# Kernel optimization log

Hardware: AMD Instinct MI355X
Metric: run time of the kernel (lower is better)

## Reference

```python
import jax, jax.numpy as jnp
import numpy as np

B, N, D, H, M = 4, 4096, 1024, 16, 128
DH = D // H
SCALE = DH ** -0.5


def setup_inputs() -> dict:
    key = jax.random.key(0)
    k1, k2, k3, k4, k5 = jax.random.split(key, 5)
    return {
        "x": jax.random.normal(k1, (B, N, D), dtype=jnp.float32),
        "agent_tokens": jax.random.normal(k2, (H, M, DH), dtype=jnp.float32) * 0.02,
        "w_fused": jax.random.normal(k3, (3 * D, D), dtype=jnp.float32) * 0.02,
        "w_qa": jax.random.normal(k4, (H, H), dtype=jnp.float32) * 0.25,
        "w_ak": jax.random.normal(k5, (H, H), dtype=jnp.float32) * 0.25,
    }


def reference(x, agent_tokens, w_fused, w_qa, w_ak):
    b, n, d = x.shape
    # Fused QKV projection (torch Linear: x @ W.T), split into q, k, v
    qkv = jnp.einsum('bnd,ed->bne', x, w_fused)  # [B, N, 3D]
    q, k, v = jnp.split(qkv, 3, axis=-1)
    # [B, N, (H dh)] -> [B, H, N, dh]
    def to_heads(t):
        return t.reshape(b, n, H, DH).transpose(0, 2, 1, 3)
    q, k, v = to_heads(q), to_heads(k), to_heads(v)
    a = agent_tokens * SCALE  # [H, M, dh], broadcast over batch
    # Stage 1 scores: query -> agents ; agents -> keys
    qa_attn = jax.nn.softmax(jnp.einsum('bhnd,hmd->bhnm', q, a), axis=-1)  # [B,H,N,M]
    ak_attn = jax.nn.softmax(jnp.einsum('hmd,bhnd->bhmn', a, k), axis=-1)  # [B,H,M,N]
    # Talking heads: 1x1 conv over head dim == HxH mixing matrix
    qa_attn = jnp.einsum('gh,bhnm->bgnm', w_qa, qa_attn)
    ak_attn = jnp.einsum('gh,bhmn->bgmn', w_ak, ak_attn)
    # Two-stage value aggregation
    agent_gathered = jnp.einsum('bhmn,bhnd->bhmd', ak_attn, v)   # [B,H,M,dh]
    out = jnp.einsum('bhnm,bhmd->bhnd', qa_attn, agent_gathered)  # [B,H,N,dh]
    return out
```

## Files before the change

kernel.cpp:

```cpp
#include <hip/hip_runtime.h>
#include <hip/hip_bf16.h>

typedef unsigned short u16;
typedef __attribute__((ext_vector_type(8))) short short8;
typedef __attribute__((ext_vector_type(4))) float f32x4;
typedef __attribute__((ext_vector_type(8))) unsigned short ushort8v;
typedef __attribute__((ext_vector_type(4))) unsigned short ushort4v;

#define DEV static __device__ __forceinline__

DEV float bf2f(u16 u) { unsigned int v = ((unsigned int)u) << 16; float f; __builtin_memcpy(&f, &v, 4); return f; }
DEV u16 f2bf(float f) { unsigned int v; __builtin_memcpy(&v, &f, 4); v += 0x7FFFu + ((v >> 16) & 1u); return (u16)(v >> 16); }

#define MFMA(a, b, c) __builtin_amdgcn_mfma_f32_16x16x32_bf16((a), (b), (c), 0, 0, 0)

#define GLOAD_LDS(g, l) __builtin_amdgcn_global_load_lds( \
    (const __attribute__((address_space(1))) unsigned int*)(g), \
    (__attribute__((address_space(3))) unsigned int*)(l), 16, 0, 0)

__global__ __launch_bounds__(256) void cvt_bf16(const float* __restrict__ in,
                                                u16* __restrict__ out, int n4) {
  int i = blockIdx.x * 256 + threadIdx.x;
  if (i >= n4) return;
  float4 v = ((const float4*)in)[i];
  ushort4v o;
  o[0] = f2bf(v.x); o[1] = f2bf(v.y); o[2] = f2bf(v.z); o[3] = f2bf(v.w);
  ((ushort4v*)out)[i] = o;
}

DEV u16* as_addr(u16* As, int row, int col) {
  int byte = (row * 64 + col * 2) ^ ((row & 7) << 4);
  return (u16*)((char*)As + byte);
}
DEV const u16* as_caddr(const u16* As, int row, int col) {
  int byte = (row * 64 + col * 2) ^ ((row & 7) << 4);
  return (const u16*)((const char*)As + byte);
}

__global__ __launch_bounds__(256, 2) void gemm_qkv(
    const float* __restrict__ X, const u16* __restrict__ W,
    u16* __restrict__ Qb, u16* __restrict__ Kb, u16* __restrict__ Vb)
{
  __shared__ u16 As[128 * 32];
  __shared__ u16 Bs[128 * 32];
  const int K = 1024;
  int t = threadIdx.x, lane = t & 63, wave = t >> 6;
  int bm = blockIdx.x, bn = blockIdx.y;

  int arow = t >> 1, acseg = (t & 1) * 16;
  const float* gx = X + (size_t)(bm * 128 + arow) * K + acseg;
  int brow = t >> 2, bcol = (t & 3) * 8;
  const u16* gb0 = W + (size_t)(bn * 128 + brow) * K + bcol;
  const u16* gb1 = gb0 + (size_t)64 * K;
  u16* lb0 = Bs + wave * 512;
  u16* lb1 = Bs + 2048 + wave * 512;

  int wm = (wave & 1) * 64, wn = (wave >> 1) * 64;
  int fr = lane & 15, fk = (lane >> 4) * 8;

  f32x4 acc[4][4];
#pragma unroll
  for (int i = 0; i < 4; ++i)
#pragma unroll
    for (int j = 0; j < 4; ++j) acc[i][j] = (f32x4){0.f, 0.f, 0.f, 0.f};

  for (int k0 = 0; k0 < K; k0 += 32) {
    GLOAD_LDS(gb0, lb0); GLOAD_LDS(gb1, lb1);
    gb0 += 32; gb1 += 32;
    float4 f0 = *(const float4*)(gx + 0);
    float4 f1 = *(const float4*)(gx + 4);
    float4 f2 = *(const float4*)(gx + 8);
    float4 f3 = *(const float4*)(gx + 12);
    gx += 32;
    ushort8v a0, a1;
    a0[0] = f2bf(f0.x); a0[1] = f2bf(f0.y); a0[2] = f2bf(f0.z); a0[3] = f2bf(f0.w);
    a0[4] = f2bf(f1.x); a0[5] = f2bf(f1.y); a0[6] = f2bf(f1.z); a0[7] = f2bf(f1.w);
    a1[0] = f2bf(f2.x); a1[1] = f2bf(f2.y); a1[2] = f2bf(f2.z); a1[3] = f2bf(f2.w);
    a1[4] = f2bf(f3.x); a1[5] = f2bf(f3.y); a1[6] = f2bf(f3.z); a1[7] = f2bf(f3.w);
    *(ushort8v*)as_addr(As, arow, acseg)     = a0;
    *(ushort8v*)as_addr(As, arow, acseg + 8) = a1;
    __syncthreads();
    short8 af[4], bfv[4];
#pragma unroll
    for (int i = 0; i < 4; ++i) af[i] = *(const short8*)as_caddr(As, wm + i * 16 + fr, fk);
#pragma unroll
    for (int j = 0; j < 4; ++j) bfv[j] = *(const short8*)&Bs[(wn + j * 16 + fr) * 32 + fk];
#pragma unroll
    for (int i = 0; i < 4; ++i)
#pragma unroll
      for (int j = 0; j < 4; ++j) acc[i][j] = MFMA(af[i], bfv[j], acc[i][j]);
    __syncthreads();
  }

  int r4 = (lane >> 4) * 4, c0 = lane & 15;
#pragma unroll
  for (int j = 0; j < 4; ++j) {
    int gcol = bn * 128 + wn + j * 16 + c0;
    int s = gcol >> 10, rem = gcol & 1023;
    int h = rem >> 6, dh = rem & 63;
    u16* dst = (s == 0) ? Qb : ((s == 1) ? Kb : Vb);
#pragma unroll
    for (int i = 0; i < 4; ++i)
#pragma unroll
      for (int r = 0; r < 4; ++r) {
        int grow = bm * 128 + wm + i * 16 + r4 + r;
        int b = grow >> 12, n = grow & 4095;
        dst[((((size_t)(b * 16 + h) << 12) | n) << 6) | dh] = f2bf(acc[i][j][r]);
      }
  }
}

__global__ __launch_bounds__(256) void qa_softmax(
    const u16* __restrict__ Qb, const float* __restrict__ At, u16* __restrict__ P1)
{
  __shared__ u16 qs[64 * 72];
  __shared__ u16 as_[128 * 72];
  int t = threadIdx.x, lane = t & 63, wave = t >> 6;
  int nb = blockIdx.x, h = blockIdx.y, b = blockIdx.z;
  const u16* qbase = Qb + ((size_t)(b * 16 + h) * 4096 + nb * 64) * 64;
  const float* abase = At + (size_t)h * 8192;
  {
    int r = t >> 2, c = (t & 3) * 16;
    *(ushort8v*)&qs[r * 72 + c]     = *(const ushort8v*)&qbase[(size_t)r * 64 + c];
    *(ushort8v*)&qs[r * 72 + c + 8] = *(const ushort8v*)&qbase[(size_t)r * 64 + c + 8];
    int ar = t >> 1, ac = (t & 1) * 32;
#pragma unroll
    for (int j = 0; j < 4; ++j) {
      float4 fa = *(const float4*)&abase[(size_t)ar * 64 + ac + j * 8];
      float4 fb = *(const float4*)&abase[(size_t)ar * 64 + ac + j * 8 + 4];
      ushort8v o;
      o[0] = f2bf(fa.x * 0.125f); o[1] = f2bf(fa.y * 0.125f);
      o[2] = f2bf(fa.z * 0.125f); o[3] = f2bf(fa.w * 0.125f);
      o[4] = f2bf(fb.x * 0.125f); o[5] = f2bf(fb.y * 0.125f);
      o[6] = f2bf(fb.z * 0.125f); o[7] = f2bf(fb.w * 0.125f);
      *(ushort8v*)&as_[ar * 72 + ac + j * 8] = o;
    }
  }
  __syncthreads();
  int fr = lane & 15, fk = (lane >> 4) * 8;
  f32x4 acc[8];
#pragma unroll
  for (int f = 0; f < 8; ++f) acc[f] = (f32x4){0.f, 0.f, 0.f, 0.f};
  short8 aq[2];
#pragma unroll
  for (int kk = 0; kk < 2; ++kk) aq[kk] = *(const short8*)&qs[(wave * 16 + fr) * 72 + kk * 32 + fk];
#pragma unroll
  for (int f = 0; f < 8; ++f) {
#pragma unroll
    for (int kk = 0; kk < 2; ++kk) {
      short8 bv = *(const short8*)&as_[(f * 16 + fr) * 72 + kk * 32 + fk];
      acc[f] = MFMA(aq[kk], bv, acc[f]);
    }
  }
#pragma unroll
  for (int r = 0; r < 4; ++r) {
    float mx = acc[0][r];
#pragma unroll
    for (int f = 1; f < 8; ++f) mx = fmaxf(mx, acc[f][r]);
#pragma unroll
    for (int d = 1; d < 16; d <<= 1) mx = fmaxf(mx, __shfl_xor(mx, d));
    float s = 0.f;
#pragma unroll
    for (int f = 0; f < 8; ++f) { float e = __expf(acc[f][r] - mx); acc[f][r] = e; s += e; }
#pragma unroll
    for (int d = 1; d < 16; d <<= 1) s += __shfl_xor(s, d);
    float inv = 1.f / s;
#pragma unroll
    for (int f = 0; f < 8; ++f) acc[f][r] *= inv;
  }
  size_t pbase = ((size_t)(b * 16 + h) * 4096 + nb * 64 + wave * 16) * 128;
#pragma unroll
  for (int f = 0; f < 8; ++f)
#pragma unroll
    for (int r = 0; r < 4; ++r)
      P1[pbase + (size_t)((lane >> 4) * 4 + r) * 128 + f * 16 + (lane & 15)] = f2bf(acc[f][r]);
}

__global__ __launch_bounds__(256) void ak_logits(
    const u16* __restrict__ Kb, const float* __restrict__ At, u16* __restrict__ L2)
{
  __shared__ u16 ks[128 * 72];
  __shared__ u16 as_[128 * 72];
  int t = threadIdx.x, lane = t & 63, wave = t >> 6;
  int nb = blockIdx.x, h = blockIdx.y, b = blockIdx.z;
  const u16* kbase = Kb + ((size_t)(b * 16 + h) * 4096 + nb * 128) * 64;
  const float* abase = At + (size_t)h * 8192;
  {
    int r = t >> 1, c = (t & 1) * 32;
#pragma unroll
    for (int j = 0; j < 4; ++j)
      *(ushort8v*)&ks[r * 72 + c + j * 8] = *(const ushort8v*)&kbase[(size_t)r * 64 + c + j * 8];
#pragma unroll
    for (int j = 0; j < 4; ++j) {
      float4 fa = *(const float4*)&abase[(size_t)r * 64 + c + j * 8];
      float4 fb = *(const float4*)&abase[(size_t)r * 64 + c + j * 8 + 4];
      ushort8v o;
      o[0] = f2bf(fa.x * 0.125f); o[1] = f2bf(fa.y * 0.125f);
      o[2] = f2bf(fa.z * 0.125f); o[3] = f2bf(fa.w * 0.125f);
      o[4] = f2bf(fb.x * 0.125f); o[5] = f2bf(fb.y * 0.125f);
      o[6] = f2bf(fb.z * 0.125f); o[7] = f2bf(fb.w * 0.125f);
      *(ushort8v*)&as_[r * 72 + c + j * 8] = o;
    }
  }
  __syncthreads();
  int fr = lane & 15, fk = (lane >> 4) * 8;
  int wm = (wave & 1) * 64, wn = (wave >> 1) * 64;
  short8 am[4][2];
#pragma unroll
  for (int mi = 0; mi < 4; ++mi)
#pragma unroll
    for (int kk = 0; kk < 2; ++kk)
      am[mi][kk] = *(const short8*)&as_[(wm + mi * 16 + fr) * 72 + kk * 32 + fk];
  f32x4 acc[4][4];
#pragma unroll
  for (int i = 0; i < 4; ++i)
#pragma unroll
    for (int j = 0; j < 4; ++j) acc[i][j] = (f32x4){0.f, 0.f, 0.f, 0.f};
#pragma unroll
  for (int nj = 0; nj < 4; ++nj) {
    short8 bk0 = *(const short8*)&ks[(wn + nj * 16 + fr) * 72 + 0 + fk];
    short8 bk1 = *(const short8*)&ks[(wn + nj * 16 + fr) * 72 + 32 + fk];
#pragma unroll
    for (int mi = 0; mi < 4; ++mi) acc[mi][nj] = MFMA(am[mi][0], bk0, acc[mi][nj]);
#pragma unroll
    for (int mi = 0; mi < 4; ++mi) acc[mi][nj] = MFMA(am[mi][1], bk1, acc[mi][nj]);
  }
  size_t rowbase = (size_t)(b * 16 + h) * 128;
#pragma unroll
  for (int mi = 0; mi < 4; ++mi)
#pragma unroll
    for (int nj = 0; nj < 4; ++nj)
#pragma unroll
      for (int r = 0; r < 4; ++r) {
        int m = wm + mi * 16 + (lane >> 4) * 4 + r;
        int n = nb * 128 + wn + nj * 16 + (lane & 15);
        L2[(rowbase + m) * 4096 + n] = f2bf(acc[mi][nj][r]);
      }
}

__global__ __launch_bounds__(256) void softmax_rows(u16* __restrict__ L)
{
  __shared__ float red[8];
  int t = threadIdx.x, lane = t & 63, wave = t >> 6;
  size_t base = (size_t)blockIdx.x * 4096;
  float v[16];
  ushort8v u0 = *(const ushort8v*)&L[base + t * 8];
  ushort8v u1 = *(const ushort8v*)&L[base + 2048 + t * 8];
#pragma unroll
  for (int j = 0; j < 8; ++j) { v[j] = bf2f(u0[j]); v[8 + j] = bf2f(u1[j]); }
  float mx = v[0];
#pragma unroll
  for (int j = 1; j < 16; ++j) mx = fmaxf(mx, v[j]);
#pragma unroll
  for (int d = 1; d < 64; d <<= 1) mx = fmaxf(mx, __shfl_xor(mx, d));
  if (lane == 0) red[wave] = mx;
  __syncthreads();
  mx = fmaxf(fmaxf(red[0], red[1]), fmaxf(red[2], red[3]));
  float s = 0.f;
#pragma unroll
  for (int j = 0; j < 16; ++j) { v[j] = __expf(v[j] - mx); s += v[j]; }
#pragma unroll
  for (int d = 1; d < 64; d <<= 1) s += __shfl_xor(s, d);
  if (lane == 0) red[4 + wave] = s;
  __syncthreads();
  float inv = 1.f / (red[4] + red[5] + red[6] + red[7]);
  ushort8v o0, o1;
#pragma unroll
  for (int j = 0; j < 8; ++j) { o0[j] = f2bf(v[j] * inv); o1[j] = f2bf(v[8 + j] * inv); }
  *(ushort8v*)&L[base + t * 8] = o0;
  *(ushort8v*)&L[base + 2048 + t * 8] = o1;
}

__global__ __launch_bounds__(256) void mix_heads(u16* __restrict__ P, const float* __restrict__ Wm)
{
  __shared__ float w[256];
  int t = threadIdx.x;
  w[t] = Wm[t];
  __syncthreads();
  int b = blockIdx.y;
  size_t pb = (size_t)b * 16 * 524288 + (size_t)blockIdx.x * 1024 + t * 4;
  float acc[16][4];
#pragma unroll
  for (int g = 0; g < 16; ++g)
#pragma unroll
    for (int j = 0; j < 4; ++j) acc[g][j] = 0.f;
  for (int hh = 0; hh < 16; ++hh) {
    ushort4v u = *(const ushort4v*)&P[pb + (size_t)hh * 524288];
    float v0 = bf2f(u[0]), v1 = bf2f(u[1]), v2 = bf2f(u[2]), v3 = bf2f(u[3]);
#pragma unroll
    for (int g = 0; g < 16; ++g) {
      float wg = w[g * 16 + hh];
      acc[g][0] += wg * v0; acc[g][1] += wg * v1;
      acc[g][2] += wg * v2; acc[g][3] += wg * v3;
    }
  }
#pragma unroll
  for (int g = 0; g < 16; ++g) {
    ushort4v o;
    o[0] = f2bf(acc[g][0]); o[1] = f2bf(acc[g][1]);
    o[2] = f2bf(acc[g][2]); o[3] = f2bf(acc[g][3]);
    *(ushort4v*)&P[pb + (size_t)g * 524288] = o;
  }
}

__global__ __launch_bounds__(256) void transpose_v(const u16* __restrict__ V, u16* __restrict__ VT)
{
  __shared__ u16 tile[64 * 72];
  int t = threadIdx.x;
  int nb = blockIdx.x, h = blockIdx.y, b = blockIdx.z;
  size_t vbase = ((size_t)(b * 16 + h) * 4096 + nb * 64) * 64;
  int r = t >> 3, c = (t & 7) * 8;
#pragma unroll
  for (int it = 0; it < 2; ++it)
    *(ushort8v*)&tile[(it * 32 + r) * 72 + c] = *(const ushort8v*)&V[vbase + (size_t)(it * 32 + r) * 64 + c];
  __syncthreads();
  size_t tbase = ((size_t)(b * 16 + h) * 64) * 4096 + nb * 64;
#pragma unroll
  for (int it = 0; it < 2; ++it) {
    int d = it * 32 + (t >> 3);
    int n8 = (t & 7) * 8;
    ushort8v o;
#pragma unroll
    for (int j = 0; j < 8; ++j) o[j] = tile[(n8 + j) * 72 + d];
    *(ushort8v*)&VT[tbase + (size_t)d * 4096 + n8] = o;
  }
}

__global__ __launch_bounds__(256) void ag_partial(
    const u16* __restrict__ P2, const u16* __restrict__ VT, float* __restrict__ agp)
{
  __shared__ u16 ps[128 * 40];
  __shared__ u16 vs[64 * 40];
  int t = threadIdx.x, lane = t & 63, wave = t >> 6;
  int ks = blockIdx.x, g = blockIdx.y, b = blockIdx.z;
  size_t pbase = (size_t)(b * 16 + g) * 128 * 4096;
  size_t vbase = (size_t)(b * 16 + g) * 64 * 4096;
  int fr = lane & 15, fk = (lane >> 4) * 8;
  int wm = (wave & 1) * 64, wd = (wave >> 1) * 32;
  int pr = t >> 1, pc = (t & 1) * 16;
  int vr = t >> 2, vc = (t & 3) * 8;
  f32x4 acc[4][2];
#pragma unroll
  for (int i = 0; i < 4; ++i)
#pragma unroll
    for (int j = 0; j < 2; ++j) acc[i][j] = (f32x4){0.f, 0.f, 0.f, 0.f};
  for (int k0 = 0; k0 < 1024; k0 += 32) {
    size_t ncol = (size_t)ks * 1024 + k0;
    *(ushort8v*)&ps[pr * 40 + pc]     = *(const ushort8v*)&P2[pbase + (size_t)pr * 4096 + ncol + pc];
    *(ushort8v*)&ps[pr * 40 + pc + 8] = *(const ushort8v*)&P2[pbase + (size_t)pr * 4096 + ncol + pc + 8];
    *(ushort8v*)&vs[vr * 40 + vc]     = *(const ushort8v*)&VT[vbase + (size_t)vr * 4096 + ncol + vc];
    __syncthreads();
    short8 am[4], bv[2];
#pragma unroll
    for (int mi = 0; mi < 4; ++mi) am[mi] = *(const short8*)&ps[(wm + mi * 16 + fr) * 40 + fk];
#pragma unroll
    for (int dj = 0; dj < 2; ++dj) bv[dj] = *(const short8*)&vs[(wd + dj * 16 + fr) * 40 + fk];
#pragma unroll
    for (int mi = 0; mi < 4; ++mi)
#pragma unroll
      for (int dj = 0; dj < 2; ++dj) acc[mi][dj] = MFMA(am[mi], bv[dj], acc[mi][dj]);
    __syncthreads();
  }
  size_t obase = ((size_t)ks * 64 + b * 16 + g) * 8192;
#pragma unroll
  for (int mi = 0; mi < 4; ++mi)
#pragma unroll
    for (int dj = 0; dj < 2; ++dj)
#pragma unroll
      for (int r = 0; r < 4; ++r) {
        int m = wm + mi * 16 + (lane >> 4) * 4 + r;
        int d = wd + dj * 16 + (lane & 15);
        agp[obase + (size_t)m * 64 + d] = acc[mi][dj][r];
      }
}

__global__ __launch_bounds__(256) void ag_reduce(const float* __restrict__ agp, u16* __restrict__ agT)
{
  size_t i = (size_t)blockIdx.x * 256 + threadIdx.x;
  float s = agp[i] + agp[i + 524288] + agp[i + 1048576] + agp[i + 1572864];
  int d = (int)(i & 63);
  int m = (int)((i >> 6) & 127);
  size_t bg = i >> 13;
  agT[(bg * 64 + d) * 128 + m] = f2bf(s);
}

__global__ __launch_bounds__(256) void out_gemm(
    const u16* __restrict__ P1, const u16* __restrict__ agT, float* __restrict__ Out)
{
  __shared__ u16 ps[128 * 136];
  __shared__ u16 gs[64 * 136];
  int t = threadIdx.x, lane = t & 63, wave = t >> 6;
  int nb = blockIdx.x, g = blockIdx.y, b = blockIdx.z;
  size_t p1base = ((size_t)(b * 16 + g) * 4096 + nb * 128) * 128;
  size_t gbase = (size_t)(b * 16 + g) * 8192;
  int r = t >> 4, c = (t & 15) * 8;
#pragma unroll
  for (int it = 0; it < 8; ++it)
    *(ushort8v*)&ps[(it * 16 + r) * 136 + c] = *(const ushort8v*)&P1[p1base + (size_t)(it * 16 + r) * 128 + c];
#pragma unroll
  for (int it = 0; it < 4; ++it)
    *(ushort8v*)&gs[(it * 16 + r) * 136 + c] = *(const ushort8v*)&agT[gbase + (size_t)(it * 16 + r) * 128 + c];
  __syncthreads();
  int fr = lane & 15, fk = (lane >> 4) * 8;
  int wm = (wave & 1) * 64, wd = (wave >> 1) * 32;
  f32x4 acc[4][2];
#pragma unroll
  for (int i = 0; i < 4; ++i)
#pragma unroll
    for (int j = 0; j < 2; ++j) acc[i][j] = (f32x4){0.f, 0.f, 0.f, 0.f};
#pragma unroll
  for (int kk = 0; kk < 4; ++kk) {
    short8 am[4], bv[2];
#pragma unroll
    for (int mi = 0; mi < 4; ++mi) am[mi] = *(const short8*)&ps[(wm + mi * 16 + fr) * 136 + kk * 32 + fk];
#pragma unroll
    for (int dj = 0; dj < 2; ++dj) bv[dj] = *(const short8*)&gs[(wd + dj * 16 + fr) * 136 + kk * 32 + fk];
#pragma unroll
    for (int mi = 0; mi < 4; ++mi)
#pragma unroll
      for (int dj = 0; dj < 2; ++dj) acc[mi][dj] = MFMA(am[mi], bv[dj], acc[mi][dj]);
  }
  size_t ob = ((size_t)(b * 16 + g) * 4096 + nb * 128) * 64;
#pragma unroll
  for (int mi = 0; mi < 4; ++mi)
#pragma unroll
    for (int dj = 0; dj < 2; ++dj)
#pragma unroll
      for (int r2 = 0; r2 < 4; ++r2) {
        int row = wm + mi * 16 + (lane >> 4) * 4 + r2;
        int col = wd + dj * 16 + (lane & 15);
        Out[ob + (size_t)row * 64 + col] = acc[mi][dj][r2];
      }
}

extern "C" void kernel_launch(void* const* d_in, const int* in_sizes, int n_in,
                              void* d_out, int out_size, void* d_ws, size_t ws_size,
                              hipStream_t stream)
{
  const float* x   = (const float*)d_in[0];
  const float* at  = (const float*)d_in[1];
  const float* wf  = (const float*)d_in[2];
  const float* wqa = (const float*)d_in[3];
  const float* wak = (const float*)d_in[4];
  float* Out = (float*)d_out;
  char* ws = (char*)d_ws;
  const size_t MB = 1ull << 20;
  u16* P1  = (u16*)(ws + 0);
  u16* wb  = (u16*)(ws + 0);
  u16* L2  = (u16*)(ws + 64 * MB);
  u16* Vb  = (u16*)(ws + 96 * MB);
  u16* Qb  = (u16*)(ws + 128 * MB);
  u16* VT  = (u16*)(ws + 128 * MB);
  u16* Kb  = (u16*)(ws + 160 * MB);
  float* agp = (float*)(ws + 160 * MB);
  u16* agT = (u16*)(ws + 168 * MB);

  cvt_bf16<<<dim3(3072), dim3(256), 0, stream>>>(wf, wb, 786432);
  gemm_qkv<<<dim3(128, 24), dim3(256), 0, stream>>>(x, wb, Qb, Kb, Vb);
  qa_softmax<<<dim3(64, 16, 4), dim3(256), 0, stream>>>(Qb, at, P1);
  transpose_v<<<dim3(64, 16, 4), dim3(256), 0, stream>>>(Vb, VT);
  ak_logits<<<dim3(32, 16, 4), dim3(256), 0, stream>>>(Kb, at, L2);
  softmax_rows<<<dim3(8192), dim3(256), 0, stream>>>(L2);
  mix_heads<<<dim3(512, 4), dim3(256), 0, stream>>>(P1, wqa);
  mix_heads<<<dim3(512, 4), dim3(256), 0, stream>>>(L2, wak);
  ag_partial<<<dim3(4, 16, 4), dim3(256), 0, stream>>>(L2, VT, agp);
  ag_reduce<<<dim3(2048), dim3(256), 0, stream>>>(agp, agT);
  out_gemm<<<dim3(32, 16, 4), dim3(256), 0, stream>>>(P1, agT, Out);
}
```

Baseline: 485.6 us.

## Pre-convert X to bf16, swizzle GEMM blocks, fuse ak softmax with head mixing

X is converted to bf16 in a separate pass so the QKV GEMM can load both operands straight into LDS with global_load_lds, dropping the per-iteration fp32 loads and conversions. The GEMM grid is flattened and block-swizzled so neighbouring blocks share tiles in L2. The separate agent-key softmax and head-mix kernels are merged into one kernel that computes per-row max and sum, then recomputes the exponentials while mixing heads, which removes one full read/write pass over the large logits buffer. The trade-offs are an extra conversion pass over X, the loss of the LDS XOR swizzle on A (possible bank conflicts), and only 512 blocks with heavy register use in the fused kernel.

```diff
diff --git a/kernel.cpp b/kernel.cpp
--- a/kernel.cpp
+++ b/kernel.cpp
@@ -28,30 +28,25 @@
   ((ushort4v*)out)[i] = o;
 }
 
-DEV u16* as_addr(u16* As, int row, int col) {
-  int byte = (row * 64 + col * 2) ^ ((row & 7) << 4);
-  return (u16*)((char*)As + byte);
-}
-DEV const u16* as_caddr(const u16* As, int row, int col) {
-  int byte = (row * 64 + col * 2) ^ ((row & 7) << 4);
-  return (const u16*)((const char*)As + byte);
-}
-
 __global__ __launch_bounds__(256, 2) void gemm_qkv(
-    const float* __restrict__ X, const u16* __restrict__ W,
+    const u16* __restrict__ X, const u16* __restrict__ W,
     u16* __restrict__ Qb, u16* __restrict__ Kb, u16* __restrict__ Vb)
 {
   __shared__ u16 As[128 * 32];
   __shared__ u16 Bs[128 * 32];
   const int K = 1024;
   int t = threadIdx.x, lane = t & 63, wave = t >> 6;
-  int bm = blockIdx.x, bn = blockIdx.y;
-
-  int arow = t >> 1, acseg = (t & 1) * 16;
-  const float* gx = X + (size_t)(bm * 128 + arow) * K + acseg;
-  int brow = t >> 2, bcol = (t & 3) * 8;
-  const u16* gb0 = W + (size_t)(bn * 128 + brow) * K + bcol;
+  int id = blockIdx.x;
+  int swz = (id & 7) * 384 + (id >> 3);
+  int bm = swz / 24, bn = swz - bm * 24;
+
+  int srow = t >> 2, scol = (t & 3) * 8;
+  const u16* ga0 = X + (size_t)(bm * 128 + srow) * K + scol;
+  const u16* ga1 = ga0 + (size_t)64 * K;
+  const u16* gb0 = W + (size_t)(bn * 128 + srow) * K + scol;
   const u16* gb1 = gb0 + (size_t)64 * K;
+  u16* la0 = As + wave * 512;
+  u16* la1 = As + 2048 + wave * 512;
   u16* lb0 = Bs + wave * 512;
   u16* lb1 = Bs + 2048 + wave * 512;
 
@@ -65,24 +60,13 @@
     for (int j = 0; j < 4; ++j) acc[i][j] = (f32x4){0.f, 0.f, 0.f, 0.f};
 
   for (int k0 = 0; k0 < K; k0 += 32) {
+    GLOAD_LDS(ga0, la0); GLOAD_LDS(ga1, la1);
     GLOAD_LDS(gb0, lb0); GLOAD_LDS(gb1, lb1);
-    gb0 += 32; gb1 += 32;
-    float4 f0 = *(const float4*)(gx + 0);
-    float4 f1 = *(const float4*)(gx + 4);
-    float4 f2 = *(const float4*)(gx + 8);
-    float4 f3 = *(const float4*)(gx + 12);
-    gx += 32;
-    ushort8v a0, a1;
-    a0[0] = f2bf(f0.x); a0[1] = f2bf(f0.y); a0[2] = f2bf(f0.z); a0[3] = f2bf(f0.w);
-    a0[4] = f2bf(f1.x); a0[5] = f2bf(f1.y); a0[6] = f2bf(f1.z); a0[7] = f2bf(f1.w);
-    a1[0] = f2bf(f2.x); a1[1] = f2bf(f2.y); a1[2] = f2bf(f2.z); a1[3] = f2bf(f2.w);
-    a1[4] = f2bf(f3.x); a1[5] = f2bf(f3.y); a1[6] = f2bf(f3.z); a1[7] = f2bf(f3.w);
-    *(ushort8v*)as_addr(As, arow, acseg)     = a0;
-    *(ushort8v*)as_addr(As, arow, acseg + 8) = a1;
+    ga0 += 32; ga1 += 32; gb0 += 32; gb1 += 32;
     __syncthreads();
     short8 af[4], bfv[4];
 #pragma unroll
-    for (int i = 0; i < 4; ++i) af[i] = *(const short8*)as_caddr(As, wm + i * 16 + fr, fk);
+    for (int i = 0; i < 4; ++i) af[i] = *(const short8*)&As[(wm + i * 16 + fr) * 32 + fk];
 #pragma unroll
     for (int j = 0; j < 4; ++j) bfv[j] = *(const short8*)&Bs[(wn + j * 16 + fr) * 32 + fk];
 #pragma unroll
@@ -238,37 +222,67 @@
       }
 }
 
-__global__ __launch_bounds__(256) void softmax_rows(u16* __restrict__ L)
-{
-  __shared__ float red[8];
-  int t = threadIdx.x, lane = t & 63, wave = t >> 6;
-  size_t base = (size_t)blockIdx.x * 4096;
-  float v[16];
-  ushort8v u0 = *(const ushort8v*)&L[base + t * 8];
-  ushort8v u1 = *(const ushort8v*)&L[base + 2048 + t * 8];
-#pragma unroll
-  for (int j = 0; j < 8; ++j) { v[j] = bf2f(u0[j]); v[8 + j] = bf2f(u1[j]); }
-  float mx = v[0];
-#pragma unroll
-  for (int j = 1; j < 16; ++j) mx = fmaxf(mx, v[j]);
-#pragma unroll
-  for (int d = 1; d < 64; d <<= 1) mx = fmaxf(mx, __shfl_xor(mx, d));
-  if (lane == 0) red[wave] = mx;
-  __syncthreads();
-  mx = fmaxf(fmaxf(red[0], red[1]), fmaxf(red[2], red[3]));
-  float s = 0.f;
-#pragma unroll
-  for (int j = 0; j < 16; ++j) { v[j] = __expf(v[j] - mx); s += v[j]; }
-#pragma unroll
-  for (int d = 1; d < 64; d <<= 1) s += __shfl_xor(s, d);
-  if (lane == 0) red[4 + wave] = s;
-  __syncthreads();
-  float inv = 1.f / (red[4] + red[5] + red[6] + red[7]);
-  ushort8v o0, o1;
-#pragma unroll
-  for (int j = 0; j < 8; ++j) { o0[j] = f2bf(v[j] * inv); o1[j] = f2bf(v[8 + j] * inv); }
-  *(ushort8v*)&L[base + t * 8] = o0;
-  *(ushort8v*)&L[base + 2048 + t * 8] = o1;
+__global__ __launch_bounds__(256) void sm_mix(u16* __restrict__ L, const float* __restrict__ Wm)
+{
+  __shared__ float w[256];
+  __shared__ float mxs[16], invs[16];
+  int t = threadIdx.x, lane = t & 63, wave = t >> 6;
+  int m = blockIdx.x, b = blockIdx.y;
+  w[t] = Wm[t];
+  const size_t HS = (size_t)128 * 4096;
+  size_t base0 = ((size_t)(b * 16) * 128 + m) * 4096;
+  for (int hh = wave; hh < 16; hh += 4) {
+    const u16* row = L + base0 + (size_t)hh * HS;
+    ushort8v vv[8];
+#pragma unroll
+    for (int it = 0; it < 8; ++it) vv[it] = *(const ushort8v*)&row[it * 512 + lane * 8];
+    float mx = -3.0e38f;
+#pragma unroll
+    for (int it = 0; it < 8; ++it)
+#pragma unroll
+      for (int j = 0; j < 8; ++j) mx = fmaxf(mx, bf2f(vv[it][j]));
+#pragma unroll
+    for (int d = 1; d < 64; d <<= 1) mx = fmaxf(mx, __shfl_xor(mx, d));
+    float s = 0.f;
+#pragma unroll
+    for (int it = 0; it < 8; ++it)
+#pragma unroll
+      for (int j = 0; j < 8; ++j) s += __expf(bf2f(vv[it][j]) - mx);
+#pragma unroll
+    for (int d = 1; d < 64; d <<= 1) s += __shfl_xor(s, d);
+    if (lane == 0) { mxs[hh] = mx; invs[hh] = 1.f / s; }
+  }
+  __syncthreads();
+#pragma unroll
+  for (int half = 0; half < 2; ++half) {
+    int n0 = t * 16 + half * 8;
+    float acc[16][8];
+#pragma unroll
+    for (int g = 0; g < 16; ++g)
+#pragma unroll
+      for (int j = 0; j < 8; ++j) acc[g][j] = 0.f;
+#pragma unroll
+    for (int hh = 0; hh < 16; ++hh) {
+      ushort8v u = *(const ushort8v*)&L[base0 + (size_t)hh * HS + n0];
+      float mxh = mxs[hh], ivh = invs[hh];
+      float p[8];
+#pragma unroll
+      for (int j = 0; j < 8; ++j) p[j] = __expf(bf2f(u[j]) - mxh) * ivh;
+#pragma unroll
+      for (int g = 0; g < 16; ++g) {
+        float wg = w[g * 16 + hh];
+#pragma unroll
+        for (int j = 0; j < 8; ++j) acc[g][j] += wg * p[j];
+      }
+    }
+#pragma unroll
+    for (int g = 0; g < 16; ++g) {
+      ushort8v o;
+#pragma unroll
+      for (int j = 0; j < 8; ++j) o[j] = f2bf(acc[g][j]);
+      *(ushort8v*)&L[base0 + (size_t)g * HS + n0] = o;
+    }
+  }
 }
 
 __global__ __launch_bounds__(256) void mix_heads(u16* __restrict__ P, const float* __restrict__ Wm)
@@ -448,6 +462,7 @@
   u16* P1  = (u16*)(ws + 0);
   u16* wb  = (u16*)(ws + 0);
   u16* L2  = (u16*)(ws + 64 * MB);
+  u16* xb  = (u16*)(ws + 64 * MB);
   u16* Vb  = (u16*)(ws + 96 * MB);
   u16* Qb  = (u16*)(ws + 128 * MB);
   u16* VT  = (u16*)(ws + 128 * MB);
@@ -455,14 +470,14 @@
   float* agp = (float*)(ws + 160 * MB);
   u16* agT = (u16*)(ws + 168 * MB);
 
-  cvt_bf16<<<dim3(3072), dim3(256), 0, stream>>>(wf, wb, 786432);
-  gemm_qkv<<<dim3(128, 24), dim3(256), 0, stream>>>(x, wb, Qb, Kb, Vb);
+  cvt_bf16<<<dim3(3072),  dim3(256), 0, stream>>>(wf, wb, 786432);
+  cvt_bf16<<<dim3(16384), dim3(256), 0, stream>>>(x, xb, 4194304);
+  gemm_qkv<<<dim3(3072), dim3(256), 0, stream>>>(xb, wb, Qb, Kb, Vb);
   qa_softmax<<<dim3(64, 16, 4), dim3(256), 0, stream>>>(Qb, at, P1);
   transpose_v<<<dim3(64, 16, 4), dim3(256), 0, stream>>>(Vb, VT);
   ak_logits<<<dim3(32, 16, 4), dim3(256), 0, stream>>>(Kb, at, L2);
-  softmax_rows<<<dim3(8192), dim3(256), 0, stream>>>(L2);
+  sm_mix<<<dim3(128, 4), dim3(256), 0, stream>>>(L2, wak);
   mix_heads<<<dim3(512, 4), dim3(256), 0, stream>>>(P1, wqa);
-  mix_heads<<<dim3(512, 4), dim3(256), 0, stream>>>(L2, wak);
   ag_partial<<<dim3(4, 16, 4), dim3(256), 0, stream>>>(L2, VT, agp);
   ag_reduce<<<dim3(2048), dim3(256), 0, stream>>>(agp, agT);
   out_gemm<<<dim3(32, 16, 4), dim3(256), 0, stream>>>(P1, agT, Out);
```

Result: slower. 534.8 us (+10.1%).
